# Optimization experiments

Measured on AMD Instinct MI355X. Metric: run time of the kernel, lower is better.

The kernel has to match this reference:

```python
import jax, jax.numpy as jnp
import numpy as np

B, T, C, K = 8, 4096, 256, 4  # batch, time, d_embd, k_periods


def setup_inputs() -> dict:
    key = jax.random.key(0)
    ks = jax.random.split(key, 5)
    x = jax.random.normal(ks[0], (B, T, C), jnp.float32)
    # inception stand-in: masked 3x3 conv (HWIO) + GELU
    Wc = jax.random.normal(ks[1], (3, 3, C, C), jnp.float32) * 0.02
    bc = jnp.zeros((C,), jnp.float32)
    # FeedForward params
    W1 = jax.random.normal(ks[2], (C, 4 * C), jnp.float32) * 0.02
    b1 = jnp.zeros((4 * C,), jnp.float32)
    W2 = jax.random.normal(ks[3], (4 * C, C), jnp.float32) * 0.02
    b2 = jnp.zeros((C,), jnp.float32)
    return {"x": x, "Wc": Wc, "bc": bc, "W1": W1, "b1": b1, "W2": W2, "b2": b2}


def _topk_freq_idx(x):
    # eager (concrete) period detection; shapes downstream are data-dependent,
    # exactly like the torch original (which is also not compilable as one graph)
    xf = jnp.fft.rfft(x, axis=1)[:, 1:, :]            # drop DC -> [B, T//2, C]
    amps_full = jnp.mean(jnp.abs(xf), axis=-1)        # [B, T//2]
    _, idx = jax.lax.top_k(amps_full, K)              # [B, K] indices into sliced bins
    return np.asarray(jax.device_get(idx))


def _fold(x, n):
    # vectorized per-sample 1D->2D folding with period n[b]; returns masked grid
    pad = (T - T % n) % n
    m = (T + pad) // n
    M, N = int(m.max()), int(n.max())
    nj = jnp.asarray(n)[:, None, None]                # [B,1,1]
    i = jnp.arange(M)[None, :, None]
    j = jnp.arange(N)[None, None, :]
    t = i * nj + j                                    # [B,M,N] flat time index
    valid = (j < nj) & (t < T)
    tc = jnp.clip(t, 0, T - 1)
    grid = x[jnp.arange(B)[:, None, None], tc] * valid[..., None]  # [B,M,N,C]
    mask = valid[..., None].astype(x.dtype)
    return grid, mask


def _inception(grid, mask, Wc, bc):
    y = jax.lax.conv_general_dilated(
        grid, Wc, window_strides=(1, 1), padding='SAME',
        dimension_numbers=('NHWC', 'HWIO', 'NHWC'))
    return jax.nn.gelu(y + bc, approximate=False) * mask


def _unfold(y, n):
    ts = jnp.arange(T)[None, :]
    nj = jnp.asarray(n)[:, None]
    return y[jnp.arange(B)[:, None], ts // nj, ts % nj]  # [B,T,C]


def _forward(x, Wc, bc, W1, b1, W2, b2, idx_np):
    # differentiable amplitude recomputation with fixed (closed-over) indices
    xf = jnp.fft.rfft(x, axis=1)[:, 1:, :]
    amps_full = jnp.mean(jnp.abs(xf), axis=-1)                     # [B, T//2]
    amps_k = jnp.take_along_axis(amps_full, jnp.asarray(idx_np), axis=1)  # [B,K]
    # original computes p = T // topk_index; clamp to avoid div-by-zero on idx 0
    p = np.maximum(T // np.maximum(idx_np, 1), 1)                   # [B,K] np ints
    outs = []
    for k in range(K):
        grid, mask = _fold(x, p[:, k])
        y = _inception(grid, mask, Wc, bc)
        outs.append(_unfold(y, p[:, k]))
    tf = jnp.stack(outs, axis=1)                                   # [B,K,T,C]
    h = jax.nn.gelu(tf @ W1 + b1, approximate=False) @ W2 + b2     # FeedForward
    w = jax.nn.softmax(amps_k, axis=-1)[:, :, None, None]
    return x + (h * w).sum(axis=1)


def reference(x, Wc, bc, W1, b1, W2, b2):
    idx_np = _topk_freq_idx(x)
    return _forward(x, Wc, bc, W1, b1, W2, b2, idx_np)
```

## Files before the change

### kernel.cpp

```cpp
#include <hip/hip_runtime.h>
#include <cstdint>
#include <cstddef>

#define T_LEN 4096
#define C_DIM 256
#define B_DIM 8
#define K_TOP 4

typedef __attribute__((ext_vector_type(8))) short bf16x8;
typedef __attribute__((ext_vector_type(4))) float f32x4;

__device__ __forceinline__ float gelu_exact(float x) {
    return 0.5f * x * (1.0f + erff(x * 0.70710678118654752f));
}

__device__ __forceinline__ unsigned short f2bf(float f) {
    uint32_t u = __float_as_uint(f);
    uint32_t r = (u + 0x7fffu + ((u >> 16) & 1u)) >> 16;
    return (unsigned short)r;
}

typedef __attribute__((address_space(3))) uint32_t lds_u32_t;
typedef __attribute__((address_space(1))) const uint32_t gbl_u32_t;

__device__ __forceinline__ void lds_load16(const void* g, void* l) {
    __builtin_amdgcn_global_load_lds((gbl_u32_t*)g, (lds_u32_t*)l, 16, 0, 0);
}

#define FPAD(i) ((i) + ((i) >> 5))

__global__ __launch_bounds__(256) void cvt_x_kernel(const float4* __restrict__ x,
                                                    float4* __restrict__ out,
                                                    ushort4* __restrict__ xbf,
                                                    unsigned short* __restrict__ zbuf) {
    size_t i = (size_t)blockIdx.x * 256 + threadIdx.x;
    float4 v = x[i];
    out[i] = v;
    ushort4 o;
    o.x = f2bf(v.x); o.y = f2bf(v.y); o.z = f2bf(v.z); o.w = f2bf(v.w);
    xbf[i] = o;
    if (blockIdx.x == 0 && threadIdx.x < 256) zbuf[threadIdx.x] = 0;
}

__global__ __launch_bounds__(256) void transpose_cvt_kernel(const float* __restrict__ src,
                                                            unsigned short* __restrict__ dst,
                                                            int R, int C) {
    __shared__ float t[32][33];
    const int c0 = blockIdx.x * 32, r0 = blockIdx.y * 32;
    const int lx = threadIdx.x & 31, ly = threadIdx.x >> 5;
    for (int rr = ly; rr < 32; rr += 8) {
        int r = r0 + rr, c = c0 + lx;
        t[rr][lx] = (r < R && c < C) ? src[(size_t)r * C + c] : 0.0f;
    }
    __syncthreads();
    for (int rr = ly; rr < 32; rr += 8) {
        int c = c0 + rr, r = r0 + lx;
        if (r < R && c < C) dst[(size_t)c * R + r] = f2bf(t[lx][rr]);
    }
}

__global__ __launch_bounds__(256) void repack_frag_kernel(const float* __restrict__ src,
                                                          unsigned short* __restrict__ dst,
                                                          int K, int N) {
    int idx = blockIdx.x * 256 + threadIdx.x;
    int total = (N >> 4) * (K >> 5) * 64;
    if (idx >= total) return;
    int lane = idx & 63, tile = idx >> 6;
    int ktiles = K >> 5;
    int tile_n = tile / ktiles, tile_k = tile % ktiles;
    int col = tile_n * 16 + (lane & 15);
    int k0 = tile_k * 32 + (lane >> 4) * 8;
    __align__(16) unsigned short v[8];
#pragma unroll
    for (int j = 0; j < 8; j++) v[j] = f2bf(src[(size_t)(k0 + j) * N + col]);
    *(uint4*)(dst + (size_t)idx * 8) = *(const uint4*)v;
}

__global__ __launch_bounds__(256) void transpose_x_kernel(const float* __restrict__ x,
                                                          float* __restrict__ xT) {
    __shared__ float tile[32][33];
    const int b = blockIdx.z;
    const int t0 = blockIdx.x * 32, c0 = blockIdx.y * 32;
    const int lx = threadIdx.x & 31, ly = threadIdx.x >> 5;
    const float* xp = x + (size_t)b * T_LEN * C_DIM;
    float* op = xT + (size_t)b * C_DIM * T_LEN;
    for (int rr = ly; rr < 32; rr += 8)
        tile[rr][lx] = xp[(size_t)(t0 + rr) * C_DIM + c0 + lx];
    __syncthreads();
    for (int rr = ly; rr < 32; rr += 8)
        op[(size_t)(c0 + rr) * T_LEN + t0 + lx] = tile[lx][rr];
}

__global__ __launch_bounds__(256) void fft_mag_kernel(const float* __restrict__ src,
                                                      float* __restrict__ mags,
                                                      int transposed) {
    const int bx = blockIdx.x;
    const int b = bx >> 8;
    const int c = bx & 255;
    const int tid = threadIdx.x;

    __shared__ __align__(16) float re[4224];
    __shared__ __align__(16) float im[4224];
    __shared__ __align__(16) float twr[2048];
    __shared__ __align__(16) float twi[2048];

    for (int u = tid; u < 2048; u += 256) {
        float ang = -6.283185307179586f * (float)u / 4096.0f;
        float s, co;
        sincosf(ang, &s, &co);
        twr[u] = co;
        twi[u] = s;
    }
    for (int i = tid; i < 4224; i += 256) im[i] = 0.0f;

    if (transposed) {
        const float4* row = (const float4*)(src + ((size_t)(b * C_DIM + c)) * T_LEN);
        for (int e4 = tid; e4 < 1024; e4 += 256) {
            float4 v = row[e4];
            int e = e4 * 4;
            re[FPAD((int)(__brev((unsigned)(e + 0)) >> 20))] = v.x;
            re[FPAD((int)(__brev((unsigned)(e + 1)) >> 20))] = v.y;
            re[FPAD((int)(__brev((unsigned)(e + 2)) >> 20))] = v.z;
            re[FPAD((int)(__brev((unsigned)(e + 3)) >> 20))] = v.w;
        }
    } else {
        const float* xp = src + (size_t)b * T_LEN * C_DIM + c;
        for (int e = tid; e < 4096; e += 256) {
            int r = (int)(__brev((unsigned)e) >> 20);
            re[FPAD(r)] = xp[(size_t)e * C_DIM];
        }
    }
    __syncthreads();

#pragma unroll
    for (int sp = 0; sp < 6; sp++) {
        const int h = 1 << (2 * sp);
        const int t1s = 11 - 2 * sp;
        const int t2s = 10 - 2 * sp;
        for (int j = tid; j < 1024; j += 256) {
            int p = j & (h - 1);
            int G = j >> (2 * sp);
            int base = G * 4 * h + p;
            int iA = FPAD(base), iB = FPAD(base + h);
            int iC = FPAD(base + 2 * h), iD = FPAD(base + 3 * h);
            float w1r = twr[p << t1s], w1i = twi[p << t1s];
            float w2r = twr[p << t2s], w2i = twi[p << t2s];
            float Ar = re[iA], Ai = im[iA], Br = re[iB], Bi = im[iB];
            float Cr = re[iC], Ci = im[iC], Dr = re[iD], Di = im[iD];
            float tBr = w1r * Br - w1i * Bi, tBi = w1r * Bi + w1i * Br;
            float tDr = w1r * Dr - w1i * Di, tDi = w1r * Di + w1i * Dr;
            float A1r = Ar + tBr, A1i = Ai + tBi;
            float B1r = Ar - tBr, B1i = Ai - tBi;
            float C1r = Cr + tDr, C1i = Ci + tDi;
            float D1r = Cr - tDr, D1i = Ci - tDi;
            float tCr = w2r * C1r - w2i * C1i, tCi = w2r * C1i + w2i * C1r;
            float uDr = w2r * D1r - w2i * D1i, uDi = w2r * D1i + w2i * D1r;
            float vDr = uDi, vDi = -uDr;
            re[iA] = A1r + tCr; im[iA] = A1i + tCi;
            re[iC] = A1r - tCr; im[iC] = A1i - tCi;
            re[iB] = B1r + vDr; im[iB] = B1i + vDi;
            re[iD] = B1r - vDr; im[iD] = B1i - vDi;
        }
        __syncthreads();
    }

    float* mp = mags + ((size_t)(b * C_DIM + c)) * 2048;
    for (int u = tid; u < 2048; u += 256) {
        int f = FPAD(u + 1);
        mp[u] = sqrtf(re[f] * re[f] + im[f] * im[f]);
    }
}

__global__ __launch_bounds__(256) void reduce_amps_kernel(const float* __restrict__ mags,
                                                          float* __restrict__ partial) {
    const int b = blockIdx.z, cc = blockIdx.y;
    const int u = blockIdx.x * 256 + threadIdx.x;
    const float* mp = mags + ((size_t)b * C_DIM + cc * 32) * 2048 + u;
    float s = 0.0f;
    for (int c = 0; c < 32; c++) s += mp[(size_t)c * 2048];
    partial[((size_t)b * 8 + cc) * 2048 + u] = s;
}

__global__ __launch_bounds__(256) void topk_kernel(const float* __restrict__ partial,
                                                   int* __restrict__ meta_p,
                                                   float* __restrict__ meta_w) {
    const int b = blockIdx.x;
    const int tid = threadIdx.x;
    __shared__ float v[2048];
    __shared__ float rv[256];
    __shared__ int ri[256];
    __shared__ float topv[K_TOP];
    __shared__ int topi[K_TOP];

    for (int u = tid; u < 2048; u += 256) {
        float s = 0.0f;
        for (int cc = 0; cc < 8; cc++) s += partial[((size_t)b * 8 + cc) * 2048 + u];
        v[u] = s * (1.0f / (float)C_DIM);
    }

    for (int k = 0; k < K_TOP; k++) {
        __syncthreads();
        float bv = -1e30f;
        int bi = 2048;
        for (int u = tid; u < 2048; u += 256) {
            float val = v[u];
            if (val > bv) { bv = val; bi = u; }
        }
        rv[tid] = bv;
        ri[tid] = bi;
        __syncthreads();
        for (int s = 128; s > 0; s >>= 1) {
            if (tid < s) {
                float ov = rv[tid + s];
                int oi = ri[tid + s];
                if (ov > rv[tid] || (ov == rv[tid] && oi < ri[tid])) {
                    rv[tid] = ov;
                    ri[tid] = oi;
                }
            }
            __syncthreads();
        }
        if (tid == 0) {
            topv[k] = rv[0];
            topi[k] = ri[0];
            v[ri[0]] = -1e30f;
        }
    }
    __syncthreads();
    if (tid == 0) {
        float mx = topv[0];
        for (int k = 1; k < K_TOP; k++) mx = fmaxf(mx, topv[k]);
        float e[K_TOP], se = 0.0f;
        for (int k = 0; k < K_TOP; k++) { e[k] = expf(topv[k] - mx); se += e[k]; }
        for (int k = 0; k < K_TOP; k++) {
            int idx = topi[k];
            int d = (idx >= 1) ? idx : 1;
            int p = T_LEN / d;
            if (p < 1) p = 1;
            meta_p[b * K_TOP + k] = p;
            meta_w[b * K_TOP + k] = e[k] / se;
        }
    }
}

__global__ __launch_bounds__(512) void conv_mfma_kernel(const unsigned short* __restrict__ xbf,
                                                        const unsigned short* __restrict__ WcT,
                                                        const float* __restrict__ bc,
                                                        const int* __restrict__ meta_p,
                                                        const unsigned short* __restrict__ zbuf,
                                                        unsigned short* __restrict__ convbufs,
                                                        size_t conv_stride, int koff) {
    const int b = blockIdx.y;
    const int kz = blockIdx.z;
    const int n = meta_p[b * K_TOP + koff + kz];
    const int row0 = blockIdx.x * 128;
    const int tid = threadIdx.x, w = tid >> 6, lane = tid & 63;
    const int wm = w >> 2, wn = w & 3;

    __shared__ __align__(16) unsigned short Al[2][128 * 32];
    __shared__ __align__(16) unsigned short Bl[2][256 * 32];

    const int ra = tid >> 2;
    const int swz = ((tid & 3) ^ (ra & 3)) * 8;
    int ti, tj;
    {
        int t = row0 + ra;
        ti = t / n;
        tj = t - ti * n;
    }
    const unsigned short* xb = xbf + (size_t)b * T_LEN * C_DIM;
    const unsigned short* baseB0 = WcT + (size_t)ra * 2304 + swz;
    const unsigned short* baseB1 = WcT + (size_t)(ra + 128) * 2304 + swz;

    auto computeA = [&](int q) -> const unsigned short* {
        int di = q / 3 - 1, dj = q % 3 - 1;
        int ii = ti + di, jj = tj + dj;
        int tp = ii * n + jj;
        bool ok = (jj >= 0) && (jj < n) && (ii >= 0) && (tp < T_LEN);
        return ok ? (xb + (size_t)tp * C_DIM + swz) : (zbuf + swz);
    };

    f32x4 acc[4][4];
#pragma unroll
    for (int m = 0; m < 4; m++)
#pragma unroll
        for (int nn = 0; nn < 4; nn++) acc[m][nn] = (f32x4){0.f, 0.f, 0.f, 0.f};

    const unsigned short* baseA = computeA(0);
    lds_load16(baseA, &Al[0][tid * 8]);
    lds_load16(baseB0, &Bl[0][tid * 8]);
    lds_load16(baseB1, &Bl[0][4096 + tid * 8]);
    __syncthreads();

#pragma unroll 2
    for (int ks = 0; ks < 72; ks++) {
        const int cur = ks & 1;
        if (ks < 71) {
            int s = ks + 1;
            if ((s & 7) == 0) baseA = computeA(s >> 3);
            lds_load16(baseA + (s & 7) * 32, &Al[cur ^ 1][tid * 8]);
            lds_load16(baseB0 + s * 32, &Bl[cur ^ 1][tid * 8]);
            lds_load16(baseB1 + s * 32, &Bl[cur ^ 1][4096 + tid * 8]);
        }

        bf16x8 af[4], bfr[4];
#pragma unroll
        for (int m = 0; m < 4; m++) {
            int row = wm * 64 + m * 16 + (lane & 15);
            af[m] = *(const bf16x8*)((const char*)&Al[cur][0] + row * 64 +
                                     (((lane >> 4) * 16) ^ ((row & 3) << 4)));
        }
#pragma unroll
        for (int nn = 0; nn < 4; nn++) {
            int rowb = wn * 64 + nn * 16 + (lane & 15);
            bfr[nn] = *(const bf16x8*)((const char*)&Bl[cur][0] + rowb * 64 +
                                       (((lane >> 4) * 16) ^ ((rowb & 3) << 4)));
        }
#pragma unroll
        for (int m = 0; m < 4; m++)
#pragma unroll
            for (int nn = 0; nn < 4; nn++)
                acc[m][nn] = __builtin_amdgcn_mfma_f32_16x16x32_bf16(af[m], bfr[nn], acc[m][nn], 0, 0, 0);

        __syncthreads();
    }

    unsigned short* ob = convbufs + (size_t)kz * conv_stride + (size_t)b * T_LEN * C_DIM;
#pragma unroll
    for (int nn = 0; nn < 4; nn++) {
        int col = wn * 64 + nn * 16 + (lane & 15);
        float bs = bc[col];
#pragma unroll
        for (int m = 0; m < 4; m++) {
            int rbase = row0 + wm * 64 + m * 16 + (lane >> 4) * 4;
#pragma unroll
            for (int r = 0; r < 4; r++) {
                float v = acc[m][nn][r] + bs;
                ob[(size_t)(rbase + r) * C_DIM + col] = f2bf(gelu_exact(v));
            }
        }
    }
}

__global__ __launch_bounds__(256, 2) void fused_ff_kernel(
    const unsigned short* __restrict__ convbufs, size_t conv_stride,
    const unsigned short* __restrict__ W1frag,
    const unsigned short* __restrict__ W2frag,
    const float* __restrict__ b1,
    const float* __restrict__ b2,
    const float* __restrict__ meta_w,
    float* __restrict__ out,
    int koff, int kcount) {
    const int tid = threadIdx.x;
    const int wn = tid >> 6, lane = tid & 63;
    const int row0 = blockIdx.x * 64;
    const int b = row0 >> 12;

    __shared__ __align__(16) unsigned short Asw[64 * 256];
    __shared__ __align__(16) unsigned short Hsw[2][64 * 128];
    __shared__ float b1s[1024];

    for (int i = tid; i < 1024; i += 256) b1s[i] = b1[i];

    f32x4 acc2[4][4];
#pragma unroll
    for (int m = 0; m < 4; m++)
#pragma unroll
        for (int nn = 0; nn < 4; nn++) acc2[m][nn] = (f32x4){0.f, 0.f, 0.f, 0.f};

    for (int kk = koff; kk < koff + kcount; kk++) {
        const float wk = meta_w[b * K_TOP + kk];
        const unsigned short* Ag =
            convbufs + (size_t)(kk - koff) * conv_stride + (size_t)row0 * C_DIM;

#pragma unroll
        for (int u = 0; u < 8; u++) {
            int ch = u * 256 + tid;
            int row = ch >> 5;
            int cole = ((ch & 31) * 8) ^ ((row & 7) << 3);
            lds_load16(Ag + (size_t)row * 256 + cole, (unsigned short*)Asw + (size_t)ch * 8);
        }
        __syncthreads();

        for (int cc = 0; cc < 8; cc++) {
            const int par = cc & 1;
            f32x4 acc1[4][2];
#pragma unroll
            for (int m = 0; m < 4; m++)
#pragma unroll
                for (int n2 = 0; n2 < 2; n2++) acc1[m][n2] = (f32x4){0.f, 0.f, 0.f, 0.f};

#pragma unroll
            for (int ks = 0; ks < 8; ks++) {
                bf16x8 af[4], bf1[2];
#pragma unroll
                for (int m = 0; m < 4; m++) {
                    int row = m * 16 + (lane & 15);
                    af[m] = *(const bf16x8*)((const char*)Asw + row * 512 +
                                             ((ks * 64 + (lane >> 4) * 16) ^ ((row & 7) << 4)));
                }
#pragma unroll
                for (int n2 = 0; n2 < 2; n2++) {
                    int tile_n = cc * 8 + wn * 2 + n2;
                    bf1[n2] = *(const bf16x8*)(W1frag + ((size_t)(tile_n * 8 + ks) * 64 + lane) * 8);
                }
#pragma unroll
                for (int m = 0; m < 4; m++)
#pragma unroll
                    for (int n2 = 0; n2 < 2; n2++)
                        acc1[m][n2] = __builtin_amdgcn_mfma_f32_16x16x32_bf16(af[m], bf1[n2],
                                                                              acc1[m][n2], 0, 0, 0);
            }

#pragma unroll
            for (int m = 0; m < 4; m++)
#pragma unroll
                for (int n2 = 0; n2 < 2; n2++) {
                    int coll = wn * 32 + n2 * 16 + (lane & 15);
                    float bb = b1s[cc * 128 + coll];
#pragma unroll
                    for (int r = 0; r < 4; r++) {
                        int row = m * 16 + (lane >> 4) * 4 + r;
                        unsigned short hv = f2bf(wk * gelu_exact(acc1[m][n2][r] + bb));
                        *(unsigned short*)((char*)&Hsw[par][0] + row * 256 +
                                           ((coll * 2) ^ ((row & 7) << 4))) = hv;
                    }
                }
            __syncthreads();

#pragma unroll
            for (int ks2 = 0; ks2 < 4; ks2++) {
                bf16x8 af2[4], bf2[4];
#pragma unroll
                for (int m = 0; m < 4; m++) {
                    int row = m * 16 + (lane & 15);
                    af2[m] = *(const bf16x8*)((const char*)&Hsw[par][0] + row * 256 +
                                              ((ks2 * 64 + (lane >> 4) * 16) ^ ((row & 7) << 4)));
                }
#pragma unroll
                for (int nn = 0; nn < 4; nn++) {
                    int tile_n = wn * 4 + nn;
                    int tile_k = cc * 4 + ks2;
                    bf2[nn] = *(const bf16x8*)(W2frag + ((size_t)(tile_n * 32 + tile_k) * 64 + lane) * 8);
                }
#pragma unroll
                for (int m = 0; m < 4; m++)
#pragma unroll
                    for (int nn = 0; nn < 4; nn++)
                        acc2[m][nn] = __builtin_amdgcn_mfma_f32_16x16x32_bf16(af2[m], bf2[nn],
                                                                              acc2[m][nn], 0, 0, 0);
            }
        }
    }

#pragma unroll
    for (int nn = 0; nn < 4; nn++) {
        int col = wn * 64 + nn * 16 + (lane & 15);
        float bb = b2[col];
#pragma unroll
        for (int m = 0; m < 4; m++) {
            int rbase = row0 + m * 16 + (lane >> 4) * 4;
#pragma unroll
            for (int r = 0; r < 4; r++)
                out[(size_t)(rbase + r) * C_DIM + col] += acc2[m][nn][r] + bb;
        }
    }
}

extern "C" void kernel_launch(void* const* d_in, const int* in_sizes, int n_in,
                              void* d_out, int out_size, void* d_ws, size_t ws_size,
                              hipStream_t stream) {
    const float* x  = (const float*)d_in[0];
    const float* Wc = (const float*)d_in[1];
    const float* bc = (const float*)d_in[2];
    const float* W1 = (const float*)d_in[3];
    const float* b1 = (const float*)d_in[4];
    const float* W2 = (const float*)d_in[5];
    const float* b2 = (const float*)d_in[6];
    float* out = (float*)d_out;

    const size_t CONV_ELEMS = (size_t)B_DIM * T_LEN * C_DIM;
    const size_t CONV_BYTES = CONV_ELEMS * 2;
    const size_t MAGS_BYTES = (size_t)B_DIM * C_DIM * 2048 * 4;
    const size_t XT_BYTES = (size_t)B_DIM * T_LEN * C_DIM * 4;

    uint8_t* ws = (uint8_t*)d_ws;
    size_t off = 0;
    auto alloc = [&](size_t bytes) {
        size_t o = off;
        off = (off + bytes + 255) & ~(size_t)255;
        return o;
    };
    float* partial = (float*)(ws + alloc((size_t)B_DIM * 8 * 2048 * 4));
    int* meta_p = (int*)(ws + alloc(B_DIM * K_TOP * 4));
    float* meta_w = (float*)(ws + alloc(B_DIM * K_TOP * 4));
    unsigned short* xbf = (unsigned short*)(ws + alloc((size_t)B_DIM * T_LEN * C_DIM * 2));
    unsigned short* WcT = (unsigned short*)(ws + alloc((size_t)256 * 2304 * 2));
    unsigned short* W1frag = (unsigned short*)(ws + alloc((size_t)256 * 1024 * 2));
    unsigned short* W2frag = (unsigned short*)(ws + alloc((size_t)1024 * 256 * 2));
    unsigned short* zbuf = (unsigned short*)(ws + alloc(512));

    size_t remaining = (ws_size > off) ? (ws_size - off) : 0;
    uint8_t* regionA = ws + off;
    int tier;
    if (remaining >= 4 * CONV_BYTES) tier = 2;
    else if (remaining >= MAGS_BYTES + XT_BYTES) tier = 1;
    else tier = 0;

    float* mags = (float*)regionA;
    float* xT = (float*)(regionA + ((tier == 2) ? CONV_BYTES : MAGS_BYTES));
    unsigned short* convbufs = (unsigned short*)regionA;
    const int use_xT = (tier >= 1);

    cvt_x_kernel<<<dim3((B_DIM * T_LEN * C_DIM / 4) / 256), 256, 0, stream>>>(
        (const float4*)x, (float4*)out, (ushort4*)xbf, zbuf);

    transpose_cvt_kernel<<<dim3(256 / 32, 2304 / 32), 256, 0, stream>>>(Wc, WcT, 2304, 256);
    repack_frag_kernel<<<dim3(128), 256, 0, stream>>>(W1, W1frag, 256, 1024);
    repack_frag_kernel<<<dim3(128), 256, 0, stream>>>(W2, W2frag, 1024, 256);

    if (use_xT) {
        transpose_x_kernel<<<dim3(T_LEN / 32, C_DIM / 32, B_DIM), 256, 0, stream>>>(x, xT);
        fft_mag_kernel<<<dim3(B_DIM * C_DIM), 256, 0, stream>>>(xT, mags, 1);
    } else {
        fft_mag_kernel<<<dim3(B_DIM * C_DIM), 256, 0, stream>>>(x, mags, 0);
    }
    reduce_amps_kernel<<<dim3(2048 / 256, 8, B_DIM), 256, 0, stream>>>(mags, partial);
    topk_kernel<<<dim3(B_DIM), 256, 0, stream>>>(partial, meta_p, meta_w);

    if (tier == 2) {
        conv_mfma_kernel<<<dim3(32, B_DIM, K_TOP), 512, 0, stream>>>(
            xbf, WcT, bc, meta_p, zbuf, convbufs, CONV_ELEMS, 0);
        fused_ff_kernel<<<dim3(B_DIM * T_LEN / 64), 256, 0, stream>>>(
            convbufs, CONV_ELEMS, W1frag, W2frag, b1, b2, meta_w, out, 0, K_TOP);
    } else {
        for (int k = 0; k < K_TOP; k++) {
            conv_mfma_kernel<<<dim3(32, B_DIM, 1), 512, 0, stream>>>(
                xbf, WcT, bc, meta_p, zbuf, convbufs, 0, k);
            fused_ff_kernel<<<dim3(B_DIM * T_LEN / 64), 256, 0, stream>>>(
                convbufs, 0, W1frag, W2frag, b1, b2, meta_w, out, k, 1);
        }
    }
}
```

Before: 452.3 us.

## Triple-buffer conv MFMA pipeline with single barrier and prefetch next FF A tile

```diff
diff --git a/kernel.cpp b/kernel.cpp
--- a/kernel.cpp
+++ b/kernel.cpp
@@ -26,6 +26,25 @@
 __device__ __forceinline__ void lds_load16(const void* g, void* l) {
     __builtin_amdgcn_global_load_lds((gbl_u32_t*)g, (lds_u32_t*)l, 16, 0, 0);
 }
+
+#define BAR_VM0()                                                      \
+    do {                                                               \
+        asm volatile("s_waitcnt vmcnt(0) lgkmcnt(0)" ::: "memory");    \
+        __builtin_amdgcn_s_barrier();                                  \
+        __builtin_amdgcn_sched_barrier(0);                             \
+    } while (0)
+#define BAR_VM3()                                                      \
+    do {                                                               \
+        asm volatile("s_waitcnt vmcnt(3) lgkmcnt(0)" ::: "memory");    \
+        __builtin_amdgcn_s_barrier();                                  \
+        __builtin_amdgcn_sched_barrier(0);                             \
+    } while (0)
+#define BAR_LGKM()                                                     \
+    do {                                                               \
+        asm volatile("s_waitcnt lgkmcnt(0)" ::: "memory");             \
+        __builtin_amdgcn_s_barrier();                                  \
+        __builtin_amdgcn_sched_barrier(0);                             \
+    } while (0)
 
 #define FPAD(i) ((i) + ((i) >> 5))
 
@@ -257,11 +276,11 @@
     const int tid = threadIdx.x, w = tid >> 6, lane = tid & 63;
     const int wm = w >> 2, wn = w & 3;
 
-    __shared__ __align__(16) unsigned short Al[2][128 * 32];
-    __shared__ __align__(16) unsigned short Bl[2][256 * 32];
+    __shared__ __align__(16) unsigned short Al[3][128 * 32];
+    __shared__ __align__(16) unsigned short Bl[3][256 * 32];
 
     const int ra = tid >> 2;
-    const int swz = ((tid & 3) ^ (ra & 3)) * 8;
+    const int swz = ((tid & 3) ^ ((ra >> 1) & 3)) * 8;
     int ti, tj;
     {
         int t = row0 + ra;
@@ -290,17 +309,21 @@
     lds_load16(baseA, &Al[0][tid * 8]);
     lds_load16(baseB0, &Bl[0][tid * 8]);
     lds_load16(baseB1, &Bl[0][4096 + tid * 8]);
-    __syncthreads();
-
-#pragma unroll 2
-    for (int ks = 0; ks < 72; ks++) {
-        const int cur = ks & 1;
-        if (ks < 71) {
-            int s = ks + 1;
-            if ((s & 7) == 0) baseA = computeA(s >> 3);
-            lds_load16(baseA + (s & 7) * 32, &Al[cur ^ 1][tid * 8]);
-            lds_load16(baseB0 + s * 32, &Bl[cur ^ 1][tid * 8]);
-            lds_load16(baseB1 + s * 32, &Bl[cur ^ 1][4096 + tid * 8]);
+    lds_load16(baseA + 32, &Al[1][tid * 8]);
+    lds_load16(baseB0 + 32, &Bl[1][tid * 8]);
+    lds_load16(baseB1 + 32, &Bl[1][4096 + tid * 8]);
+
+    int cur = 0, stb = 2;
+    for (int s = 0; s < 72; s++) {
+        if (s < 71) BAR_VM3();
+        else        BAR_VM0();
+
+        const int t = s + 2;
+        if (t < 72) {
+            if ((t & 7) == 0) baseA = computeA(t >> 3);
+            lds_load16(baseA + (t & 7) * 32, &Al[stb][tid * 8]);
+            lds_load16(baseB0 + (size_t)t * 32, &Bl[stb][tid * 8]);
+            lds_load16(baseB1 + (size_t)t * 32, &Bl[stb][4096 + tid * 8]);
         }
 
         bf16x8 af[4], bfr[4];
@@ -308,13 +331,13 @@
         for (int m = 0; m < 4; m++) {
             int row = wm * 64 + m * 16 + (lane & 15);
             af[m] = *(const bf16x8*)((const char*)&Al[cur][0] + row * 64 +
-                                     (((lane >> 4) * 16) ^ ((row & 3) << 4)));
+                                     (((lane >> 4) * 16) ^ (((row >> 1) & 3) << 4)));
         }
 #pragma unroll
         for (int nn = 0; nn < 4; nn++) {
             int rowb = wn * 64 + nn * 16 + (lane & 15);
             bfr[nn] = *(const bf16x8*)((const char*)&Bl[cur][0] + rowb * 64 +
-                                       (((lane >> 4) * 16) ^ ((rowb & 3) << 4)));
+                                       (((lane >> 4) * 16) ^ (((rowb >> 1) & 3) << 4)));
         }
 #pragma unroll
         for (int m = 0; m < 4; m++)
@@ -322,7 +345,8 @@
             for (int nn = 0; nn < 4; nn++)
                 acc[m][nn] = __builtin_amdgcn_mfma_f32_16x16x32_bf16(af[m], bfr[nn], acc[m][nn], 0, 0, 0);
 
-        __syncthreads();
+        cur = (cur == 2) ? 0 : cur + 1;
+        stb = (stb == 2) ? 0 : stb + 1;
     }
 
     unsigned short* ob = convbufs + (size_t)kz * conv_stride + (size_t)b * T_LEN * C_DIM;
@@ -360,19 +384,7 @@
     __shared__ __align__(16) unsigned short Hsw[2][64 * 128];
     __shared__ float b1s[1024];
 
-    for (int i = tid; i < 1024; i += 256) b1s[i] = b1[i];
-
-    f32x4 acc2[4][4];
-#pragma unroll
-    for (int m = 0; m < 4; m++)
-#pragma unroll
-        for (int nn = 0; nn < 4; nn++) acc2[m][nn] = (f32x4){0.f, 0.f, 0.f, 0.f};
-
-    for (int kk = koff; kk < koff + kcount; kk++) {
-        const float wk = meta_w[b * K_TOP + kk];
-        const unsigned short* Ag =
-            convbufs + (size_t)(kk - koff) * conv_stride + (size_t)row0 * C_DIM;
-
+    auto stageA = [&](const unsigned short* Ag) {
 #pragma unroll
         for (int u = 0; u < 8; u++) {
             int ch = u * 256 + tid;
@@ -380,7 +392,21 @@
             int cole = ((ch & 31) * 8) ^ ((row & 7) << 3);
             lds_load16(Ag + (size_t)row * 256 + cole, (unsigned short*)Asw + (size_t)ch * 8);
         }
-        __syncthreads();
+    };
+
+    for (int i = tid; i < 1024; i += 256) b1s[i] = b1[i];
+
+    f32x4 acc2[4][4];
+#pragma unroll
+    for (int m = 0; m < 4; m++)
+#pragma unroll
+        for (int nn = 0; nn < 4; nn++) acc2[m][nn] = (f32x4){0.f, 0.f, 0.f, 0.f};
+
+    stageA(convbufs + (size_t)row0 * C_DIM);
+
+    for (int kk = koff; kk < koff + kcount; kk++) {
+        BAR_VM0();
+        const float wk = meta_w[b * K_TOP + kk];
 
         for (int cc = 0; cc < 8; cc++) {
             const int par = cc & 1;
@@ -426,7 +452,10 @@
                                            ((coll * 2) ^ ((row & 7) << 4))) = hv;
                     }
                 }
-            __syncthreads();
+            BAR_LGKM();
+
+            if (cc == 7 && kk + 1 < koff + kcount)
+                stageA(convbufs + (size_t)(kk + 1 - koff) * conv_stride + (size_t)row0 * C_DIM);
 
 #pragma unroll
             for (int ks2 = 0; ks2 < 4; ks2++) {
```

After: 461.3 us. Within noise of the previous version (+2.0%).
